# Kernel tuning notes

Measured on AMD Instinct MI355X. Metric: run time of the kernel, lower is better.

Reference implementation:

```python
import jax, jax.numpy as jnp
import numpy as np

N = 8192
F_IN = 1024
F_OUT = 256
ALPHA = 0.2          # LeakyReLU negative slope
ADJ_DENSITY = 0.004  # pre-symmetrization edge probability -> avg degree ~65
NEG_INF = -9.0e15    # matches -9000000000000000.0 in the torch code


def setup_inputs() -> dict:
    key = jax.random.key(0)
    k_h, k_W, k_a, k_adj = jax.random.split(key, 4)
    h = jax.random.normal(k_h, (N, F_IN), dtype=jnp.float32)
    # xavier_uniform with gain=1.414
    lim_W = 1.414 * np.sqrt(6.0 / (F_IN + F_OUT))
    W = jax.random.uniform(k_W, (F_IN, F_OUT), dtype=jnp.float32, minval=-lim_W, maxval=lim_W)
    lim_a = 1.414 * np.sqrt(6.0 / (2 * F_OUT + 1))
    a = jax.random.uniform(k_a, (2 * F_OUT, 1), dtype=jnp.float32, minval=-lim_a, maxval=lim_a)
    # sparse symmetric 0/1 adjacency (float, like the torch code's dense adj)
    u = jax.random.uniform(k_adj, (N, N))
    m = u < ADJ_DENSITY
    adj = (m | m.T).astype(jnp.float32)
    return {"h": h, "adj": adj, "W": W, "a": a}


def reference(h, adj, W, a):
    # --- GAT attention ---
    Wh = h @ W                                   # [N, F_OUT]
    Wh1 = Wh @ a[:F_OUT]                          # [N, 1]
    Wh2 = Wh @ a[F_OUT:]                          # [N, 1]
    e = jax.nn.leaky_relu(Wh1 + Wh2.T, negative_slope=ALPHA)   # [N, N]
    attention = jax.nn.softmax(jnp.where(adj > 0, e, NEG_INF), axis=1)

    # --- per-row variable-k pruning of attention + attention@attention.T ---
    n = adj.shape[0]
    diag = jnp.eye(n, dtype=bool)
    adj_nodiag = jnp.where(diag, 0.0, adj)
    s2 = jnp.count_nonzero(adj_nodiag, axis=1)    # [N] int, variable k per row

    attention2step = attention @ attention.T      # [N, N] dense GEMM
    comb = attention + attention2step
    comb = jnp.where(diag, 0.0, comb)

    # threshold = s2[i]-th largest value of row i (np.partition(row, -k)[-k])
    sorted_desc = -jnp.sort(-comb, axis=1)        # [N, N] descending per row
    idx = jnp.maximum(s2 - 1, 0)[:, None]         # clamp for s2==0 rows
    thr = jnp.take_along_axis(sorted_desc, idx, axis=1)   # [N, 1]
    # keep values >= threshold (torch code zeros values strictly < partition);
    # rows with s2 == 0 are zeroed entirely
    pruned = jnp.where((s2[:, None] > 0) & (comb >= thr), comb, 0.0)
    adj_resize = (pruned > 0).astype(jnp.float32)

    # --- output (eval mode: dropout is identity); concat=True -> ELU ---
    h_prime = attention @ Wh                      # [N, F_OUT]
    return jax.nn.elu(h_prime), adj_resize
```

## Files before the change

### kernel.cpp

```cpp
#include <hip/hip_runtime.h>
#include <cstdint>
#include <cstddef>

#define NN 8192
#define KFIN 1024
#define KFOUT 256
#define MAXD 192
#define LRALPHA 0.2f

typedef float f32x4 __attribute__((ext_vector_type(4)));

__global__ void __launch_bounds__(256) k_csr_gemm(
    const float* __restrict__ adj, int* __restrict__ nbr,
    int* __restrict__ deg, int* __restrict__ s2v,
    const float* __restrict__ A, const float* __restrict__ B,
    float* __restrict__ C) {
  __shared__ float As[16][65];
  __shared__ float Bs[16][65];
  if (blockIdx.x < 2048) {
    const int wave = threadIdx.x >> 6;
    const int lane = threadIdx.x & 63;
    const int row = blockIdx.x * 4 + wave;
    const float* arow = adj + (size_t)row * NN;
    int* outp = nbr + (size_t)row * MAXD;
    int count = 0;
    int dflag = 0;
    const unsigned long long below = (1ull << lane) - 1ull;
    for (int c0 = 0; c0 < NN; c0 += 256) {
      const int c = c0 + lane * 4;
      const f32x4 v = __builtin_nontemporal_load(
          reinterpret_cast<const f32x4*>(arow + c));
      const unsigned long long m0 = __ballot(v[0] > 0.0f);
      const unsigned long long m1 = __ballot(v[1] > 0.0f);
      const unsigned long long m2 = __ballot(v[2] > 0.0f);
      const unsigned long long m3 = __ballot(v[3] > 0.0f);
      int pos = count + (int)(__popcll(m0 & below) + __popcll(m1 & below) +
                              __popcll(m2 & below) + __popcll(m3 & below));
      if (v[0] > 0.0f) { if (pos < MAXD) outp[pos] = c + 0; ++pos; if (c + 0 == row) dflag = 1; }
      if (v[1] > 0.0f) { if (pos < MAXD) outp[pos] = c + 1; ++pos; if (c + 1 == row) dflag = 1; }
      if (v[2] > 0.0f) { if (pos < MAXD) outp[pos] = c + 2; ++pos; if (c + 2 == row) dflag = 1; }
      if (v[3] > 0.0f) { if (pos < MAXD) outp[pos] = c + 3; ++pos; if (c + 3 == row) dflag = 1; }
      count += (int)(__popcll(m0) + __popcll(m1) + __popcll(m2) + __popcll(m3));
    }
    const int anyd = __any(dflag) ? 1 : 0;
    if (lane == 0) {
      deg[row] = count < MAXD ? count : MAXD;
      s2v[row] = count - anyd;
    }
    return;
  }
  const int bx = blockIdx.x - 2048;
  const int tid = threadIdx.x;
  const int brow = (bx >> 2) * 64;
  const int bcol = (bx & 3) * 64;
  const int tx = tid & 15;
  const int ty = tid >> 4;
  float acc[4][4];
#pragma unroll
  for (int i = 0; i < 4; ++i)
#pragma unroll
    for (int j = 0; j < 4; ++j) acc[i][j] = 0.0f;
  const int ar = tid >> 2;
  const int ac = (tid & 3) << 2;
  const int br = tid >> 4;
  const int bc = (tid & 15) << 2;
  for (int k0 = 0; k0 < KFIN; k0 += 16) {
    const float4 av =
        *reinterpret_cast<const float4*>(A + (size_t)(brow + ar) * KFIN + k0 + ac);
    const float4 bv =
        *reinterpret_cast<const float4*>(B + (size_t)(k0 + br) * KFOUT + bcol + bc);
    As[ac + 0][ar] = av.x;
    As[ac + 1][ar] = av.y;
    As[ac + 2][ar] = av.z;
    As[ac + 3][ar] = av.w;
    Bs[br][bc + 0] = bv.x;
    Bs[br][bc + 1] = bv.y;
    Bs[br][bc + 2] = bv.z;
    Bs[br][bc + 3] = bv.w;
    __syncthreads();
#pragma unroll
    for (int kk = 0; kk < 16; ++kk) {
      const float a0 = As[kk][ty * 4 + 0];
      const float a1 = As[kk][ty * 4 + 1];
      const float a2 = As[kk][ty * 4 + 2];
      const float a3 = As[kk][ty * 4 + 3];
      const float b0 = Bs[kk][tx * 4 + 0];
      const float b1 = Bs[kk][tx * 4 + 1];
      const float b2 = Bs[kk][tx * 4 + 2];
      const float b3 = Bs[kk][tx * 4 + 3];
      acc[0][0] += a0 * b0; acc[0][1] += a0 * b1; acc[0][2] += a0 * b2; acc[0][3] += a0 * b3;
      acc[1][0] += a1 * b0; acc[1][1] += a1 * b1; acc[1][2] += a1 * b2; acc[1][3] += a1 * b3;
      acc[2][0] += a2 * b0; acc[2][1] += a2 * b1; acc[2][2] += a2 * b2; acc[2][3] += a2 * b3;
      acc[3][0] += a3 * b0; acc[3][1] += a3 * b1; acc[3][2] += a3 * b2; acc[3][3] += a3 * b3;
    }
    __syncthreads();
  }
#pragma unroll
  for (int i = 0; i < 4; ++i) {
#pragma unroll
    for (int j = 0; j < 4; ++j) {
      C[(size_t)(brow + ty * 4 + i) * KFOUT + bcol + tx * 4 + j] = acc[i][j];
    }
  }
}

__global__ void __launch_bounds__(256) k_rowdots(
    const float* __restrict__ Wh, const float* __restrict__ a,
    float* __restrict__ Wh1, float* __restrict__ Wh2) {
  __shared__ float sA[256];
  __shared__ float sB[256];
  const int row = blockIdx.x;
  const int t = threadIdx.x;
  const float w = Wh[(size_t)row * KFOUT + t];
  sA[t] = w * a[t];
  sB[t] = w * a[KFOUT + t];
  __syncthreads();
  for (int s = 128; s > 0; s >>= 1) {
    if (t < s) {
      sA[t] += sA[t + s];
      sB[t] += sB[t + s];
    }
    __syncthreads();
  }
  if (t == 0) {
    Wh1[row] = sA[0];
    Wh2[row] = sB[0];
  }
}

__global__ void __launch_bounds__(256) k_stats(
    const int* __restrict__ nbr, const int* __restrict__ deg,
    const float* __restrict__ Wh1, const float* __restrict__ Wh2,
    float* __restrict__ mrow, float* __restrict__ Zrow) {
  const int wave = threadIdx.x >> 6;
  const int lane = threadIdx.x & 63;
  const int row = blockIdx.x * 4 + wave;
  const int d = deg[row];
  const int* cols = nbr + (size_t)row * MAXD;
  const float w1 = Wh1[row];
  float mx = -1e30f;
  for (int t = lane; t < d; t += 64) {
    float e = w1 + Wh2[cols[t]];
    e = e > 0.0f ? e : LRALPHA * e;
    mx = fmaxf(mx, e);
  }
  for (int o = 32; o > 0; o >>= 1) mx = fmaxf(mx, __shfl_xor(mx, o));
  float sum = 0.0f;
  for (int t = lane; t < d; t += 64) {
    float e = w1 + Wh2[cols[t]];
    e = e > 0.0f ? e : LRALPHA * e;
    sum += expf(e - mx);
  }
  for (int o = 32; o > 0; o >>= 1) sum += __shfl_xor(sum, o);
  if (lane == 0) {
    mrow[row] = mx;
    Zrow[row] = (d > 0) ? sum : 1.0f;
  }
}

__global__ void __launch_bounds__(256) k_att(
    const int* __restrict__ nbr, const int* __restrict__ deg,
    const float* __restrict__ Wh1, const float* __restrict__ Wh2,
    const float* __restrict__ mrow, const float* __restrict__ Zrow,
    float* __restrict__ att, int2* __restrict__ edgesT,
    short* __restrict__ qb8) {
  const int wave = threadIdx.x >> 6;
  const int lane = threadIdx.x & 63;
  const int row = blockIdx.x * 4 + wave;
  const int d = deg[row];
  const int* cols = nbr + (size_t)row * MAXD;
  const float w1r = Wh1[row];
  const float w2r = Wh2[row];
  const float mr = mrow[row];
  const float invZr = 1.0f / Zrow[row];
  int b[7] = {0, 0, 0, 0, 0, 0, 0};
  for (int t0 = 0; t0 < d; t0 += 64) {
    const int t = t0 + lane;
    const bool act = t < d;
    const int j = act ? cols[t] : 0x7fffffff;
#pragma unroll
    for (int m = 1; m <= 7; ++m)
      b[m - 1] += (int)__popcll(__ballot(act && j < m * 1024));
    if (act) {
      float e = w1r + Wh2[j];
      e = e > 0.0f ? e : LRALPHA * e;
      att[(size_t)row * MAXD + t] = expf(e - mr) * invZr;
      float e2 = Wh1[j] + w2r;
      e2 = e2 > 0.0f ? e2 : LRALPHA * e2;
      const float v = expf(e2 - mrow[j]) / Zrow[j];
      edgesT[(size_t)row * MAXD + t] = make_int2(j, __float_as_int(v));
    }
  }
  if (lane == 0) {
    short* q = qb8 + (size_t)row * 8;
    q[0] = (short)b[0]; q[1] = (short)b[1]; q[2] = (short)b[2]; q[3] = (short)b[3];
    q[4] = (short)b[4]; q[5] = (short)b[5]; q[6] = (short)b[6]; q[7] = (short)d;
  }
}

__global__ void __launch_bounds__(512) k_twostep(
    const int* __restrict__ nbr, const int* __restrict__ deg,
    const int* __restrict__ s2v, const float* __restrict__ att,
    const int2* __restrict__ edgesT, const short* __restrict__ qb8,
    float* __restrict__ out1) {
  __shared__ float comb[NN];
  __shared__ float wvals[MAXD];
  __shared__ int kcols[MAXD];
  __shared__ int kbase[MAXD];
  __shared__ unsigned short packw[8][MAXD];
  __shared__ unsigned int hist[256];
  __shared__ unsigned int shPrefix;
  __shared__ int shRemaining;
  const int tid = threadIdx.x;
  const int wave = tid >> 6;
  const int lane = tid & 63;
  const int row = blockIdx.x;
  const f32x4 z4 = {0.0f, 0.0f, 0.0f, 0.0f};
  for (int j = tid * 4; j < NN; j += 2048)
    *reinterpret_cast<f32x4*>(&comb[j]) = z4;
  const int d = deg[row];
  const int* cols = nbr + (size_t)row * MAXD;
  const float* arow = att + (size_t)row * MAXD;
  for (int t = tid; t < d; t += 512) {
    const int c = cols[t];
    kcols[t] = c;
    kbase[t] = c * MAXD;
    wvals[t] = arow[t];
  }
  for (int tt = tid; tt < d * 8; tt += 512) {
    const int t = tt >> 3;
    const int w = tt & 7;
    const int c = cols[t];
    const int qe = (int)qb8[(size_t)c * 8 + w];
    const int qs = w ? (int)qb8[(size_t)c * 8 + w - 1] : 0;
    packw[w][t] = (unsigned short)(qs | (qe << 8));
  }
  __syncthreads();
  {
    const int grp = lane >> 4;
    const int sub = lane & 15;
    const int nsteps = (d + 3) >> 2;
    int2 eA = make_int2(0, 0), eB = make_int2(0, 0);
    int2 eC = make_int2(0, 0), eD = make_int2(0, 0);
    float wA = 0.0f, wB = 0.0f, wC = 0.0f, wD = 0.0f;
    bool pA_ = false, pB_ = false, pC_ = false, pD_ = false;
#define PA_ISSUE(E_, W_, P_, S_)                                       \
    {                                                                   \
      const int t_ = (S_) * 4 + grp;                                    \
      const bool v_ = t_ < d;                                           \
      const unsigned pk_ = v_ ? (unsigned)packw[wave][t_] : 0u;         \
      const int qs_ = (int)(pk_ & 255u);                                \
      const int qe_ = (int)(pk_ >> 8);                                  \
      P_ = v_ && (qs_ + sub) < qe_;                                     \
      W_ = v_ ? wvals[t_] : 0.0f;                                       \
      E_ = make_int2(0, 0);                                             \
      if (P_) E_ = edgesT[(size_t)kbase[t_] + qs_ + sub];               \
    }
    if (nsteps > 0) PA_ISSUE(eA, wA, pA_, 0);
    if (nsteps > 1) PA_ISSUE(eB, wB, pB_, 1);
    if (nsteps > 2) PA_ISSUE(eC, wC, pC_, 2);
    if (nsteps > 3) PA_ISSUE(eD, wD, pD_, 3);
    for (int s = 0; s < nsteps; ++s) {
      const int2 e = eA; const float w = wA; const bool p = pA_;
      eA = eB; wA = wB; pA_ = pB_;
      eB = eC; wB = wC; pB_ = pC_;
      eC = eD; wC = wD; pC_ = pD_;
      if (s + 4 < nsteps) PA_ISSUE(eD, wD, pD_, s + 4);
      if (p) atomicAdd(&comb[e.x], w * __int_as_float(e.y));
    }
#undef PA_ISSUE
  }
  for (int t0 = 0; t0 < d; t0 += 64) {
    const int t = t0 + lane;
    bool big = false;
    if (t < d) {
      const unsigned pk = (unsigned)packw[wave][t];
      big = ((int)(pk >> 8) - (int)(pk & 255u)) > 16;
    }
    unsigned long long m = __ballot(big);
    while (m) {
      const int tt = t0 + (int)__ffsll((long long)m) - 1;
      m &= m - 1;
      const unsigned pk = (unsigned)packw[wave][tt];
      const int qs = (int)(pk & 255u);
      const int qe = (int)(pk >> 8);
      const float w = wvals[tt];
      const int base = kbase[tt];
      for (int off = qs + 16 + lane; off < qe; off += 64) {
        const int2 e = edgesT[(size_t)base + off];
        atomicAdd(&comb[e.x], w * __int_as_float(e.y));
      }
    }
  }
  {
    const short* qr = qb8 + (size_t)row * 8;
    const int qlo = wave ? (int)qr[wave - 1] : 0;
    const int qhi = (int)qr[wave];
    for (int t = qlo + lane; t < qhi; t += 64) comb[kcols[t]] += wvals[t];
  }
  __syncthreads();
  if (tid == 0) comb[row] = 0.0f;
  __syncthreads();
  const int kk = s2v[row];
  const size_t obase = (size_t)row * NN;
  if (kk <= 0) {
    for (int j = tid * 4; j < NN; j += 2048)
      __builtin_nontemporal_store(z4, reinterpret_cast<f32x4*>(&out1[obase + j]));
    return;
  }
  unsigned int prefix = 0u;
  int remaining = kk;
  for (int pass = 0; pass < 4; ++pass) {
    const int shift = 24 - 8 * pass;
    const unsigned int pmask = (pass == 0) ? 0u : (0xFFFFFFFFu << (shift + 8));
    if (tid < 256) hist[tid] = 0u;
    __syncthreads();
    for (int j = tid * 4; j < NN; j += 2048) {
      const f32x4 cv = *reinterpret_cast<const f32x4*>(&comb[j]);
#pragma unroll
      for (int q = 0; q < 4; ++q) {
        const unsigned int u = __float_as_uint(cv[q]);
        if (u != 0u && (u & pmask) == prefix)
          atomicAdd(&hist[(u >> shift) & 255u], 1u);
      }
    }
    __syncthreads();
    if (tid < 64) {
      const int bHi = 255 - 4 * lane;
      const unsigned int c0 = hist[bHi];
      const unsigned int c1 = hist[bHi - 1];
      const unsigned int c2 = hist[bHi - 2];
      const unsigned int c3 = hist[bHi - 3];
      const unsigned int gs = c0 + c1 + c2 + c3;
      unsigned int run2 = gs;
      for (int o = 1; o < 64; o <<= 1) {
        const unsigned int tt = __shfl_up(run2, o);
        if (lane >= o) run2 += tt;
      }
      const unsigned int pre = run2 - gs;
      const unsigned int rem = (unsigned int)remaining;
      if (pre < rem && pre + gs >= rem) {
        unsigned int above;
        int digit;
        if (pre + c0 >= rem) { digit = bHi; above = pre; }
        else if (pre + c0 + c1 >= rem) { digit = bHi - 1; above = pre + c0; }
        else if (pre + c0 + c1 + c2 >= rem) { digit = bHi - 2; above = pre + c0 + c1; }
        else { digit = bHi - 3; above = pre + c0 + c1 + c2; }
        shPrefix = prefix | ((unsigned int)digit << shift);
        shRemaining = remaining - (int)above;
      }
    }
    __syncthreads();
    prefix = shPrefix;
    remaining = shRemaining;
    __syncthreads();
  }
  const float thr = __uint_as_float(prefix);
  for (int j = tid * 4; j < NN; j += 2048) {
    const f32x4 cv = *reinterpret_cast<const f32x4*>(&comb[j]);
    f32x4 ov;
    ov[0] = (cv[0] >= thr && cv[0] > 0.0f) ? 1.0f : 0.0f;
    ov[1] = (cv[1] >= thr && cv[1] > 0.0f) ? 1.0f : 0.0f;
    ov[2] = (cv[2] >= thr && cv[2] > 0.0f) ? 1.0f : 0.0f;
    ov[3] = (cv[3] >= thr && cv[3] > 0.0f) ? 1.0f : 0.0f;
    __builtin_nontemporal_store(ov, reinterpret_cast<f32x4*>(&out1[obase + j]));
  }
}

__global__ void __launch_bounds__(256) k_hprime(
    const int* __restrict__ nbr, const int* __restrict__ deg,
    const float* __restrict__ att, const float* __restrict__ Wh,
    float* __restrict__ out0) {
  __shared__ int scol[MAXD];
  __shared__ float sval[MAXD];
  const int row = blockIdx.x;
  const int c = threadIdx.x;
  const int d = deg[row];
  const int* cols = nbr + (size_t)row * MAXD;
  const float* arow = att + (size_t)row * MAXD;
  for (int t = threadIdx.x; t < d; t += 256) {
    scol[t] = cols[t];
    sval[t] = arow[t];
  }
  __syncthreads();
  float a0 = 0.0f, a1 = 0.0f, a2 = 0.0f, a3 = 0.0f;
  int t = 0;
  for (; t + 4 <= d; t += 4) {
    a0 += sval[t + 0] * Wh[(size_t)scol[t + 0] * KFOUT + c];
    a1 += sval[t + 1] * Wh[(size_t)scol[t + 1] * KFOUT + c];
    a2 += sval[t + 2] * Wh[(size_t)scol[t + 2] * KFOUT + c];
    a3 += sval[t + 3] * Wh[(size_t)scol[t + 3] * KFOUT + c];
  }
  for (; t < d; ++t) a0 += sval[t] * Wh[(size_t)scol[t] * KFOUT + c];
  const float acc = (a0 + a1) + (a2 + a3);
  out0[(size_t)row * KFOUT + c] = acc > 0.0f ? acc : expm1f(acc);
}

extern "C" void kernel_launch(void* const* d_in, const int* in_sizes, int n_in,
                              void* d_out, int out_size, void* d_ws, size_t ws_size,
                              hipStream_t stream) {
  const float* h = (const float*)d_in[0];
  const float* adj = (const float*)d_in[1];
  const float* W = (const float*)d_in[2];
  const float* a = (const float*)d_in[3];

  float* out0 = (float*)d_out;
  float* out1 = out0 + (size_t)NN * KFOUT;

  float* Wh = (float*)d_ws;
  float* Wh1 = Wh + (size_t)NN * KFOUT;
  float* Wh2 = Wh1 + NN;
  float* mrow = Wh2 + NN;
  float* Zrow = mrow + NN;
  float* att = Zrow + NN;
  float* edgesF = att + (size_t)NN * MAXD;
  int2* edgesT = (int2*)edgesF;
  int* nbr = (int*)(edgesF + (size_t)NN * MAXD * 2);
  int* deg = nbr + (size_t)NN * MAXD;
  int* s2v = deg + NN;
  short* qb8 = (short*)(s2v + NN);

  k_csr_gemm<<<2048 + 512, 256, 0, stream>>>(adj, nbr, deg, s2v, h, W, Wh);
  k_rowdots<<<NN, 256, 0, stream>>>(Wh, a, Wh1, Wh2);
  k_stats<<<NN / 4, 256, 0, stream>>>(nbr, deg, Wh1, Wh2, mrow, Zrow);
  k_att<<<NN / 4, 256, 0, stream>>>(nbr, deg, Wh1, Wh2, mrow, Zrow, att, edgesT, qb8);
  k_twostep<<<NN, 512, 0, stream>>>(nbr, deg, s2v, att, edgesT, qb8, out1);
  k_hprime<<<NN, 256, 0, stream>>>(nbr, deg, att, Wh, out0);
}
```

Baseline: 544.6 us.

## Split CSR build from GEMM and aggregate first-pass radix histogram atomics per wave

The fused CSR-build/GEMM launch is split into two separate kernels, with the GEMM now using a 2D grid. Running them serially drops the overlap between the bandwidth-bound adjacency scan and the compute-bound GEMM. In the top-k radix select, the first histogram pass now groups lanes that share a bin via ballot/shfl, so a single leader issues one atomicAdd per bin. This is meant to cut shared-memory atomic contention, since many values share the top exponent byte, at the cost of a serial loop over the distinct bins in each wave.

```diff
diff --git a/kernel.cpp b/kernel.cpp
--- a/kernel.cpp
+++ b/kernel.cpp
@@ -10,49 +10,48 @@
 
 typedef float f32x4 __attribute__((ext_vector_type(4)));
 
-__global__ void __launch_bounds__(256) k_csr_gemm(
+__global__ void __launch_bounds__(256) k_build_csr(
     const float* __restrict__ adj, int* __restrict__ nbr,
-    int* __restrict__ deg, int* __restrict__ s2v,
+    int* __restrict__ deg, int* __restrict__ s2v) {
+  const int wave = threadIdx.x >> 6;
+  const int lane = threadIdx.x & 63;
+  const int row = blockIdx.x * 4 + wave;
+  const float* arow = adj + (size_t)row * NN;
+  int* outp = nbr + (size_t)row * MAXD;
+  int count = 0;
+  int dflag = 0;
+  const unsigned long long below = (1ull << lane) - 1ull;
+  for (int c0 = 0; c0 < NN; c0 += 256) {
+    const int c = c0 + lane * 4;
+    const f32x4 v = __builtin_nontemporal_load(
+        reinterpret_cast<const f32x4*>(arow + c));
+    const unsigned long long m0 = __ballot(v[0] > 0.0f);
+    const unsigned long long m1 = __ballot(v[1] > 0.0f);
+    const unsigned long long m2 = __ballot(v[2] > 0.0f);
+    const unsigned long long m3 = __ballot(v[3] > 0.0f);
+    int pos = count + (int)(__popcll(m0 & below) + __popcll(m1 & below) +
+                            __popcll(m2 & below) + __popcll(m3 & below));
+    if (v[0] > 0.0f) { if (pos < MAXD) outp[pos] = c + 0; ++pos; if (c + 0 == row) dflag = 1; }
+    if (v[1] > 0.0f) { if (pos < MAXD) outp[pos] = c + 1; ++pos; if (c + 1 == row) dflag = 1; }
+    if (v[2] > 0.0f) { if (pos < MAXD) outp[pos] = c + 2; ++pos; if (c + 2 == row) dflag = 1; }
+    if (v[3] > 0.0f) { if (pos < MAXD) outp[pos] = c + 3; ++pos; if (c + 3 == row) dflag = 1; }
+    count += (int)(__popcll(m0) + __popcll(m1) + __popcll(m2) + __popcll(m3));
+  }
+  const int anyd = __any(dflag) ? 1 : 0;
+  if (lane == 0) {
+    deg[row] = count < MAXD ? count : MAXD;
+    s2v[row] = count - anyd;
+  }
+}
+
+__global__ void __launch_bounds__(256) k_gemm(
     const float* __restrict__ A, const float* __restrict__ B,
     float* __restrict__ C) {
   __shared__ float As[16][65];
   __shared__ float Bs[16][65];
-  if (blockIdx.x < 2048) {
-    const int wave = threadIdx.x >> 6;
-    const int lane = threadIdx.x & 63;
-    const int row = blockIdx.x * 4 + wave;
-    const float* arow = adj + (size_t)row * NN;
-    int* outp = nbr + (size_t)row * MAXD;
-    int count = 0;
-    int dflag = 0;
-    const unsigned long long below = (1ull << lane) - 1ull;
-    for (int c0 = 0; c0 < NN; c0 += 256) {
-      const int c = c0 + lane * 4;
-      const f32x4 v = __builtin_nontemporal_load(
-          reinterpret_cast<const f32x4*>(arow + c));
-      const unsigned long long m0 = __ballot(v[0] > 0.0f);
-      const unsigned long long m1 = __ballot(v[1] > 0.0f);
-      const unsigned long long m2 = __ballot(v[2] > 0.0f);
-      const unsigned long long m3 = __ballot(v[3] > 0.0f);
-      int pos = count + (int)(__popcll(m0 & below) + __popcll(m1 & below) +
-                              __popcll(m2 & below) + __popcll(m3 & below));
-      if (v[0] > 0.0f) { if (pos < MAXD) outp[pos] = c + 0; ++pos; if (c + 0 == row) dflag = 1; }
-      if (v[1] > 0.0f) { if (pos < MAXD) outp[pos] = c + 1; ++pos; if (c + 1 == row) dflag = 1; }
-      if (v[2] > 0.0f) { if (pos < MAXD) outp[pos] = c + 2; ++pos; if (c + 2 == row) dflag = 1; }
-      if (v[3] > 0.0f) { if (pos < MAXD) outp[pos] = c + 3; ++pos; if (c + 3 == row) dflag = 1; }
-      count += (int)(__popcll(m0) + __popcll(m1) + __popcll(m2) + __popcll(m3));
-    }
-    const int anyd = __any(dflag) ? 1 : 0;
-    if (lane == 0) {
-      deg[row] = count < MAXD ? count : MAXD;
-      s2v[row] = count - anyd;
-    }
-    return;
-  }
-  const int bx = blockIdx.x - 2048;
   const int tid = threadIdx.x;
-  const int brow = (bx >> 2) * 64;
-  const int bcol = (bx & 3) * 64;
+  const int brow = blockIdx.y * 64;
+  const int bcol = blockIdx.x * 64;
   const int tx = tid & 15;
   const int ty = tid >> 4;
   float acc[4][4];
@@ -315,13 +314,34 @@
     const unsigned int pmask = (pass == 0) ? 0u : (0xFFFFFFFFu << (shift + 8));
     if (tid < 256) hist[tid] = 0u;
     __syncthreads();
-    for (int j = tid * 4; j < NN; j += 2048) {
-      const f32x4 cv = *reinterpret_cast<const f32x4*>(&comb[j]);
-#pragma unroll
-      for (int q = 0; q < 4; ++q) {
-        const unsigned int u = __float_as_uint(cv[q]);
-        if (u != 0u && (u & pmask) == prefix)
-          atomicAdd(&hist[(u >> shift) & 255u], 1u);
+    if (pass == 0) {
+      for (int j = tid * 4; j < NN; j += 2048) {
+        const f32x4 cv = *reinterpret_cast<const f32x4*>(&comb[j]);
+#pragma unroll
+        for (int q = 0; q < 4; ++q) {
+          const unsigned int u = __float_as_uint(cv[q]);
+          const bool act = (u != 0u);
+          const unsigned int bin = u >> 24;
+          unsigned long long mask = __ballot(act);
+          while (mask) {
+            const int leader = (int)__ffsll((long long)mask) - 1;
+            const unsigned int lbin = __shfl(bin, leader);
+            const unsigned long long same = __ballot(act && bin == lbin);
+            if (lane == leader)
+              atomicAdd(&hist[lbin], (unsigned int)__popcll(same));
+            mask &= ~same;
+          }
+        }
+      }
+    } else {
+      for (int j = tid * 4; j < NN; j += 2048) {
+        const f32x4 cv = *reinterpret_cast<const f32x4*>(&comb[j]);
+#pragma unroll
+        for (int q = 0; q < 4; ++q) {
+          const unsigned int u = __float_as_uint(cv[q]);
+          if (u != 0u && (u & pmask) == prefix)
+            atomicAdd(&hist[(u >> shift) & 255u], 1u);
+        }
       }
     }
     __syncthreads();
@@ -420,7 +440,9 @@
   int* s2v = deg + NN;
   short* qb8 = (short*)(s2v + NN);
 
-  k_csr_gemm<<<2048 + 512, 256, 0, stream>>>(adj, nbr, deg, s2v, h, W, Wh);
+  k_build_csr<<<NN / 4, 256, 0, stream>>>(adj, nbr, deg, s2v);
+  dim3 ggrid(KFOUT / 64, NN / 64);
+  k_gemm<<<ggrid, 256, 0, stream>>>(h, W, Wh);
   k_rowdots<<<NN, 256, 0, stream>>>(Wh, a, Wh1, Wh2);
   k_stats<<<NN / 4, 256, 0, stream>>>(nbr, deg, Wh1, Wh2, mrow, Zrow);
   k_att<<<NN / 4, 256, 0, stream>>>(nbr, deg, Wh1, Wh2, mrow, Zrow, att, edgesT, qb8);
```

After: 647.9 us. 19.0% more time.
